# Kernel tuning notes

Measured on AMD Instinct MI355X. Metric: run time of the kernel, lower is better.

Reference implementation:

```python
import jax, jax.numpy as jnp
import numpy as np

SEQ_LEN = 2048   # configs.seq_len == h == KFSSM H
PRED_LEN = 720   # configs.pred_len == p
D_MODEL = 128    # configs.d_model == KFSSM N (complex state size N//2)
C_OUT = 64       # configs.c_out == channel dim of u
BATCH = 128


def setup_inputs() -> dict:
    key = jax.random.key(0)
    ks = jax.random.split(key, 12)
    H, n2, p = SEQ_LEN, D_MODEL // 2, PRED_LEN
    u = jax.random.normal(ks[0], (BATCH, SEQ_LEN, C_OUT), jnp.float32)
    x_mark_enc = jax.random.normal(ks[1], (BATCH, SEQ_LEN, 4), jnp.float32)
    x_dec = jax.random.normal(ks[2], (BATCH, PRED_LEN, C_OUT), jnp.float32)
    x_mark_dec = jax.random.normal(ks[3], (BATCH, PRED_LEN, 4), jnp.float32)
    # standard-normal noise; scaled by learned std inside reference (matches torch.normal(0, std))
    W_noise = jax.random.normal(ks[4], (BATCH, SEQ_LEN, C_OUT), jnp.float32)
    # Model params
    D = jax.random.normal(ks[5], (H,), jnp.float32)
    log_variance = jnp.log(1.0 + jax.random.uniform(ks[6], (1,), jnp.float32))
    # KFSSM params
    C_param = jax.random.normal(ks[7], (H, n2, 2), jnp.float32)  # view_as_real of complex C
    log_dt = (jax.random.uniform(ks[8], (H,), jnp.float32)
              * (np.log(0.1) - np.log(0.001)) + np.log(0.001))
    log_A_real = jnp.log(0.5 * jnp.ones((H, n2), jnp.float32))
    A_imag = np.pi * jnp.tile(jnp.arange(n2, dtype=jnp.float32)[None, :], (H, 1))
    # outporj: Linear(h -> 2p) then GLU(dim=2)
    proj_w = jax.random.normal(ks[9], (2 * p, H), jnp.float32) * 0.02
    proj_b = jnp.zeros((2 * p,), jnp.float32)
    return dict(u=u, x_mark_enc=x_mark_enc, x_dec=x_dec, x_mark_dec=x_mark_dec,
                W_noise=W_noise, D=D, log_variance=log_variance, C_param=C_param,
                log_dt=log_dt, log_A_real=log_A_real, A_imag=A_imag,
                proj_w=proj_w, proj_b=proj_b)


def _ssm_kernels(Nl, C_param, log_dt, log_A_real, A_imag):
    # KFSSM.forward(N=Nl): returns K, K2 of shape (H, Nl)
    dt = jnp.exp(log_dt)                              # (H,)
    C = C_param[..., 0] + 1j * C_param[..., 1]        # (H, n2)
    A = -jnp.exp(log_A_real) + 1j * A_imag            # (H, n2)
    ar = jnp.arange(Nl, dtype=log_dt.dtype)
    Bk = A[:, :1] * ar[None, :] * dt[:, None]         # (H, Nl) complex
    dtA = A * dt[:, None]                             # (H, n2)
    Kexp = jnp.exp(dtA[:, :, None] * ar[None, None, :])  # (H, n2, Nl)
    Cc = C * (jnp.exp(dtA) - 1.0) / A                 # (H, n2)
    K = 2.0 * jnp.einsum('hn,hnl->hl', Cc, Kexp).real # (H, Nl)
    K2 = 2.0 * (K * Bk).real                          # (H, Nl)
    return K, K2


def reference(u, x_mark_enc, x_dec, x_mark_dec, W_noise, D, log_variance,
              C_param, log_dt, log_A_real, A_imag, proj_w, proj_b):
    # instance normalization over time
    x_mean = jnp.mean(u, axis=1, keepdims=True)                  # (B,1,N)
    u0 = u - x_mean
    x_var = jnp.var(u0, axis=1, ddof=1, keepdims=True) + 1e-5    # unbiased, as torch.var
    un = u0 / jnp.sqrt(x_var)
    # Kalman process noise
    std = jnp.sqrt(jnp.exp(log_variance))                        # (1,)
    W = std * W_noise                                            # (B,L,N)
    l, Nch = un.shape[1], un.shape[2]
    nfft = 2 * l
    K, K2 = _ssm_kernels(Nch, C_param, log_dt, log_A_real, A_imag)  # (H=l, Nch)
    k_f = jnp.fft.rfft(K.T, n=nfft, axis=-1)                     # (Nch, l+1)
    k2_f = jnp.fft.rfft(K2.T, n=nfft, axis=-1)
    u_f = jnp.fft.rfft(jnp.transpose(un, (0, 2, 1)), n=nfft, axis=-1)   # (B,Nch,l+1)
    w_f = jnp.fft.rfft(jnp.transpose(W, (0, 2, 1)), n=nfft, axis=-1)
    y = (jnp.fft.irfft(u_f * k2_f, n=nfft, axis=-1)
         + jnp.fft.irfft(w_f * k_f, n=nfft, axis=-1))            # (B,Nch,2l)
    y = jnp.transpose(y, (0, 2, 1))[:, -l:, :] + un * D[:, None] # (B,l,Nch)
    # outporj: Linear(h->2p) over time axis, then GLU(dim=2); Dropout1d is identity at eval
    z = jnp.einsum('bnh,ph->bnp', jnp.transpose(y, (0, 2, 1)), proj_w) + proj_b  # (B,Nch,2p)
    a, b = jnp.split(z, 2, axis=2)
    y = jnp.transpose(a * jax.nn.sigmoid(b), (0, 2, 1))          # (B,p,Nch)
    y = y * jnp.sqrt(x_var) + x_mean
    return y[:, -PRED_LEN:, :]
```

## Files before the change

kernel.cpp:

```cpp
#include <hip/hip_runtime.h>
#include <math.h>

typedef unsigned short u16;
typedef unsigned int u32;
typedef __attribute__((ext_vector_type(8))) short short8;
typedef __attribute__((ext_vector_type(4))) float f32x4;

#define B_   128
#define L_   2048
#define C_   64
#define P_   720
#define P2_  1440
#define NPAD 1536
#define NFFT 4096
#define NROW (B_*C_)
#define TCHUNK 16

__device__ __forceinline__ u16 f2bf(float f) {
  union { float f; unsigned u; } x; x.f = f;
  unsigned r = x.u + 0x7fffu + ((x.u >> 16) & 1u);
  return (u16)(r >> 16);
}
__device__ __forceinline__ float bf2f_lo(u32 v) {
  union { unsigned u; float f; } x; x.u = v << 16; return x.f;
}
__device__ __forceinline__ float bf2f_hi(u32 v) {
  union { unsigned u; float f; } x; x.u = v & 0xffff0000u; return x.f;
}

__device__ __forceinline__ float2 cmul(float2 a, float2 b) {
  return make_float2(a.x * b.x - a.y * b.y, a.x * b.y + a.y * b.x);
}
__device__ __forceinline__ float2 cadd(float2 a, float2 b) { return make_float2(a.x + b.x, a.y + b.y); }
__device__ __forceinline__ float2 csub(float2 a, float2 b) { return make_float2(a.x - b.x, a.y - b.y); }

#define CSWAP(i, j) { float2 tt = a[i]; a[i] = a[j]; a[j] = tt; }

template<bool INV, bool HZ>
__device__ __forceinline__ void dft16(float2 a[16]) {
  const float S  = INV ? 1.f : -1.f;
  const float c1 = 0.9238795325112867f, s1 = 0.3826834323650898f, q2 = 0.7071067811865476f;
  const float2 W1 = make_float2( c1, S * s1), W2 = make_float2( q2, S * q2), W3 = make_float2( s1, S * c1);
  const float2 W5 = make_float2(-s1, S * c1), W6 = make_float2(-q2, S * q2), W7 = make_float2(-c1, S * s1);
  if (HZ) {
    a[8]  = a[0];
    a[9]  = cmul(a[1], W1);
    a[10] = cmul(a[2], W2);
    a[11] = cmul(a[3], W3);
    a[12] = make_float2(-S * a[4].y, S * a[4].x);
    a[13] = cmul(a[5], W5);
    a[14] = cmul(a[6], W6);
    a[15] = cmul(a[7], W7);
  } else {
    float2 t;
    t = csub(a[0], a[8]);  a[0] = cadd(a[0], a[8]);  a[8]  = t;
    t = csub(a[1], a[9]);  a[1] = cadd(a[1], a[9]);  a[9]  = cmul(t, W1);
    t = csub(a[2], a[10]); a[2] = cadd(a[2], a[10]); a[10] = cmul(t, W2);
    t = csub(a[3], a[11]); a[3] = cadd(a[3], a[11]); a[11] = cmul(t, W3);
    t = csub(a[4], a[12]); a[4] = cadd(a[4], a[12]); a[12] = make_float2(-S * t.y, S * t.x);
    t = csub(a[5], a[13]); a[5] = cadd(a[5], a[13]); a[13] = cmul(t, W5);
    t = csub(a[6], a[14]); a[6] = cadd(a[6], a[14]); a[14] = cmul(t, W6);
    t = csub(a[7], a[15]); a[7] = cadd(a[7], a[15]); a[15] = cmul(t, W7);
  }
#pragma unroll
  for (int h = 0; h < 16; h += 8) {
    float2 t;
    t = csub(a[h+0], a[h+4]); a[h+0] = cadd(a[h+0], a[h+4]); a[h+4] = t;
    t = csub(a[h+1], a[h+5]); a[h+1] = cadd(a[h+1], a[h+5]); a[h+5] = cmul(t, W2);
    t = csub(a[h+2], a[h+6]); a[h+2] = cadd(a[h+2], a[h+6]); a[h+6] = make_float2(-S * t.y, S * t.x);
    t = csub(a[h+3], a[h+7]); a[h+3] = cadd(a[h+3], a[h+7]); a[h+7] = cmul(t, W6);
  }
#pragma unroll
  for (int q = 0; q < 16; q += 4) {
    float2 t;
    t = csub(a[q+0], a[q+2]); a[q+0] = cadd(a[q+0], a[q+2]); a[q+2] = t;
    t = csub(a[q+1], a[q+3]); a[q+1] = cadd(a[q+1], a[q+3]); a[q+3] = make_float2(-S * t.y, S * t.x);
  }
#pragma unroll
  for (int p = 0; p < 16; p += 2) {
    float2 t = csub(a[p], a[p+1]); a[p] = cadd(a[p], a[p+1]); a[p+1] = t;
  }
  CSWAP(1, 8); CSWAP(2, 4); CSWAP(3, 12); CSWAP(5, 10); CSWAP(7, 14); CSWAP(11, 13);
}

__device__ __forceinline__ void twchain(float2 a[16], float2 w1) {
  float2 w2 = cmul(w1, w1);
  float2 w3 = cmul(w2, w1);
  float2 w4 = cmul(w2, w2);
  float2 w5 = cmul(w3, w2);
  float2 w6 = cmul(w3, w3);
  float2 w7 = cmul(w4, w3);
  float2 w8 = cmul(w4, w4);
  float2 w9 = cmul(w5, w4);
  float2 w10 = cmul(w5, w5);
  float2 w11 = cmul(w6, w5);
  float2 w12 = cmul(w6, w6);
  float2 w13 = cmul(w7, w6);
  float2 w14 = cmul(w7, w7);
  float2 w15 = cmul(w8, w7);
  a[1]  = cmul(a[1],  w1);  a[2]  = cmul(a[2],  w2);  a[3]  = cmul(a[3],  w3);
  a[4]  = cmul(a[4],  w4);  a[5]  = cmul(a[5],  w5);  a[6]  = cmul(a[6],  w6);
  a[7]  = cmul(a[7],  w7);  a[8]  = cmul(a[8],  w8);  a[9]  = cmul(a[9],  w9);
  a[10] = cmul(a[10], w10); a[11] = cmul(a[11], w11); a[12] = cmul(a[12], w12);
  a[13] = cmul(a[13], w13); a[14] = cmul(a[14], w14); a[15] = cmul(a[15], w15);
}

__device__ __forceinline__ void lds_wA(float2* X, const float2 r[16], int tid) {
  int base = (tid & 15) * 16 + ((tid >> 4) ^ ((tid & 7) << 1));
#pragma unroll
  for (int i = 0; i < 16; ++i) X[base + i * 256] = r[i];
}
__device__ __forceinline__ void lds_wB(float2* X, const float2 r[16], int tid) {
#pragma unroll
  for (int i = 0; i < 16; ++i)
    X[((tid & 0xF0) + i) * 16 + ((tid & 15) ^ ((i & 7) << 1))] = r[i];
}
__device__ __forceinline__ void lds_rd(const float2* X, float2 r[16], int tid) {
  const float4* X4 = (const float4*)X;
#pragma unroll
  for (int p = 0; p < 8; ++p) {
    float4 v = X4[tid * 8 + (p ^ (tid & 7))];
    r[2 * p]     = make_float2(v.x, v.y);
    r[2 * p + 1] = make_float2(v.z, v.w);
  }
}

__device__ __forceinline__ void fft_fwd_hz(float2 r[16], float2* X, int tid, const float2* twg) {
  dft16<false, true>(r);
  twchain(r, twg[tid]);
  lds_wA(X, r, tid);
  __syncthreads();
  lds_rd(X, r, tid);
  dft16<false, false>(r);
  twchain(r, twg[(tid & 15) << 4]);
  __syncthreads();
  lds_wB(X, r, tid);
  __syncthreads();
  lds_rd(X, r, tid);
  dft16<false, false>(r);
}

__device__ __forceinline__ void fft_inv(float2 r[16], float2* X, int tid, const float2* twg) {
  dft16<true, false>(r);
  __syncthreads();
  lds_wB(X, r, tid);
  __syncthreads();
  lds_rd(X, r, tid);
  float2 wb = twg[(tid & 15) << 4];
  twchain(r, make_float2(wb.x, -wb.y));
  dft16<true, false>(r);
  __syncthreads();
  lds_wA(X, r, tid);
  __syncthreads();
  lds_rd(X, r, tid);
  float2 wa = twg[tid];
  twchain(r, make_float2(wa.x, -wa.y));
  dft16<true, false>(r);
}

__global__ void k_twfill(float2* __restrict__ tw) {
  int k = threadIdx.x;
  double ang = -2.0 * 3.14159265358979323846 * (double)k / 4096.0;
  tw[k] = make_float2((float)cos(ang), (float)sin(ang));
}

__global__ void k_wconv(const float* __restrict__ pw, u16* __restrict__ wb) {
  size_t idx = (size_t)blockIdx.x * 256 + threadIdx.x;
  int n = (int)(idx >> 11);
  int k = (int)(idx & 2047);
  float v = (n < P2_) ? pw[(size_t)n * L_ + k] : 0.0f;
  wb[idx] = f2bf(v);
}

__global__ __launch_bounds__(256) void k_stats1(const float* __restrict__ u, float* __restrict__ ps,
                                                float* __restrict__ pq) {
  int blk = blockIdx.x;
  int b = blk >> 4, q = blk & 15;
  int tid = threadIdx.x;
  int c4 = tid & 15, g = tid >> 4;
  const float4* u4 = (const float4*)(u + ((size_t)b * L_ + q * 128) * C_);
  float4 s = make_float4(0.f, 0.f, 0.f, 0.f), sq = s;
#pragma unroll
  for (int i = 0; i < 8; ++i) {
    float4 v = u4[(size_t)(g + 16 * i) * 16 + c4];
    s.x += v.x; s.y += v.y; s.z += v.z; s.w += v.w;
    sq.x += v.x * v.x; sq.y += v.y * v.y; sq.z += v.z * v.z; sq.w += v.w * v.w;
  }
  __shared__ float4 sb[16][16], qb[16][16];
  sb[g][c4] = s; qb[g][c4] = sq;
  __syncthreads();
  if (g == 0) {
    float4 S = sb[0][c4], Q = qb[0][c4];
#pragma unroll
    for (int k = 1; k < 16; ++k) {
      float4 a = sb[k][c4], d = qb[k][c4];
      S.x += a.x; S.y += a.y; S.z += a.z; S.w += a.w;
      Q.x += d.x; Q.y += d.y; Q.z += d.z; Q.w += d.w;
    }
    ((float4*)ps)[blk * 16 + c4] = S;
    ((float4*)pq)[blk * 16 + c4] = Q;
  }
}

__global__ __launch_bounds__(256) void k_stats2(const float* __restrict__ ps, const float* __restrict__ pq,
                                                float4* __restrict__ mv) {
  int gid = blockIdx.x * 256 + threadIdx.x;
  int b = gid >> 6, c = gid & 63;
  float S = 0.f, Q = 0.f;
#pragma unroll
  for (int q = 0; q < 16; ++q) {
    S += ps[(size_t)(b * 16 + q) * 64 + c];
    Q += pq[(size_t)(b * 16 + q) * 64 + c];
  }
  float mean = S * (1.0f / 2048.0f);
  float var = (Q - S * S * (1.0f / 2048.0f)) * (1.0f / 2047.0f) + 1e-5f;
  float sv = sqrtf(var);
  mv[gid] = make_float4(mean, sv, 1.0f / sv, 0.0f);
}

__global__ __launch_bounds__(256) void k_ssmk(const float* __restrict__ Cp, const float* __restrict__ ldt,
                                              const float* __restrict__ lAr, const float* __restrict__ Aim,
                                              float2* __restrict__ kz) {
  int gid = blockIdx.x * 256 + threadIdx.x;
  int h = gid & 2047;
  int j = gid >> 11;
  float dt = expf(ldt[h]);
  float accx = 0.f;
  float Ar0 = 0.f;
  for (int n = 0; n < 64; ++n) {
    float Ar = -expf(lAr[h * 64 + n]);
    float Ai = Aim[h * 64 + n];
    if (n == 0) Ar0 = Ar;
    float dAr = Ar * dt, dAi = Ai * dt;
    float er = expf(dAr);
    float s1, c1; sincosf(dAi, &s1, &c1);
    float emr = er * c1 - 1.0f, emi = er * s1;
    float inv = 1.0f / (Ar * Ar + Ai * Ai);
    float qr = (emr * Ar + emi * Ai) * inv;
    float qi = (emi * Ar - emr * Ai) * inv;
    float cr = Cp[(size_t)(h * 64 + n) * 2];
    float ci = Cp[(size_t)(h * 64 + n) * 2 + 1];
    float ccr = cr * qr - ci * qi;
    float cci = cr * qi + ci * qr;
    float ej = expf(dAr * (float)j);
    float sj, cj; sincosf(dAi * (float)j, &sj, &cj);
    accx += ccr * (ej * cj) - cci * (ej * sj);
  }
  float K = 2.0f * accx;
  float K2 = 2.0f * K * (Ar0 * (float)j * dt);
  kz[(size_t)j * L_ + h] = make_float2(K2, -K);
}

__global__ __launch_bounds__(256) void k_packT(const float* __restrict__ u, const float* __restrict__ Wn,
                                               const float* __restrict__ lv, const float4* __restrict__ mv,
                                               u32* __restrict__ zu) {
  int b = blockIdx.x >> 5;
  int t0 = (blockIdx.x & 31) << 6;
  int tid = threadIdx.x;
  float stdn = sqrtf(__expf(lv[0]));
  __shared__ float2 tile[64][65];
  int c = tid & 63, r = tid >> 6;
  float4 m = mv[b * C_ + c];
#pragma unroll
  for (int i = 0; i < 16; ++i) {
    int t = t0 + i * 4 + r;
    size_t idx = ((size_t)b * L_ + t) * C_ + c;
    float uu = (u[idx] - m.x) * m.z;
    float ww = Wn[idx] * stdn;
    tile[i * 4 + r][c] = make_float2(uu, ww);
  }
  __syncthreads();
  int t = tid & 63, cb = tid >> 6;
#pragma unroll
  for (int i = 0; i < 16; ++i) {
    int c2 = i * 4 + cb;
    float2 v = tile[t][c2];
    zu[((size_t)(b * C_ + c2)) * L_ + t0 + t] = ((u32)f2bf(v.y) << 16) | (u32)f2bf(v.x);
  }
}

__global__ __launch_bounds__(256) void k_fftk(const float2* __restrict__ kz, const float2* __restrict__ twg,
                                              float2* __restrict__ G) {
  __shared__ float2 X[NFFT];
  int j = blockIdx.x, tid = threadIdx.x;
  float2 r[16];
#pragma unroll
  for (int n2 = 0; n2 < 8; ++n2) r[n2] = kz[(size_t)j * L_ + n2 * 256 + tid];
  fft_fwd_hz(r, X, tid, twg);
  const float sc = 1.0f / 8192.0f;
#pragma unroll
  for (int k0 = 0; k0 < 16; ++k0)
    G[(size_t)j * NFFT + k0 * 256 + tid] = make_float2(r[k0].x * sc, r[k0].y * sc);
}

__global__ __launch_bounds__(256) void k_fftmain(const u32* __restrict__ zu, const float2* __restrict__ twg,
                                                 const float2* __restrict__ G, const float* __restrict__ Dv,
                                                 u16* __restrict__ yT) {
  __shared__ float2 X[NFFT];
  int pair = blockIdx.x;
  int b = pair >> 5, j1 = pair & 31, j2 = j1 + 32;
  int row1 = b * 64 + j1, row2 = b * 64 + j2;
  int tid = threadIdx.x;
  float2 r[16], Y1[16];
  float usav1[8], usav2[8];
#pragma unroll
  for (int n2 = 0; n2 < 8; ++n2) {
    u32 v = zu[(size_t)row1 * L_ + n2 * 256 + tid];
    r[n2] = make_float2(bf2f_lo(v), bf2f_hi(v));
    usav1[n2] = r[n2].x;
  }
  fft_fwd_hz(r, X, tid, twg);
  const float2* G1 = G + (size_t)j1 * NFFT;
#pragma unroll
  for (int k0 = 0; k0 < 16; ++k0) Y1[k0] = cmul(r[k0], G1[k0 * 256 + tid]);
  __syncthreads();
#pragma unroll
  for (int n2 = 0; n2 < 8; ++n2) {
    u32 v = zu[(size_t)row2 * L_ + n2 * 256 + tid];
    r[n2] = make_float2(bf2f_lo(v), bf2f_hi(v));
    usav2[n2] = r[n2].x;
  }
  fft_fwd_hz(r, X, tid, twg);
  const float2* G2 = G + (size_t)j2 * NFFT;
#pragma unroll
  for (int k0 = 0; k0 < 16; ++k0) r[k0] = cmul(r[k0], G2[k0 * 256 + tid]);
  __syncthreads();
  int rr = (tid & 15) * 16 + (tid >> 4);
  int wsw = ((rr & 15) << 4) | (rr >> 4);
  int rp = (tid == 0) ? 0 : 256 - rr;
  int rsw = ((rp & 15) << 4) | (rp >> 4);
#pragma unroll
  for (int k0 = 0; k0 < 16; ++k0) {
    X[k0 * 256 + wsw] = make_float2(Y1[k0].x + r[k0].y, r[k0].x - Y1[k0].y);
  }
  __syncthreads();
#pragma unroll
  for (int k0 = 0; k0 < 16; ++k0) {
    int k0p = (tid == 0) ? ((16 - k0) & 15) : (15 - k0);
    float2 Tm = X[k0p * 256 + rsw];
    r[k0] = make_float2(Y1[k0].x - r[k0].y + Tm.x, Y1[k0].y + r[k0].x + Tm.y);
  }
  fft_inv(r, X, tid, twg);
#pragma unroll
  for (int n2 = 8; n2 < 16; ++n2) {
    int t = (n2 - 8) * 256 + tid;
    float d = Dv[t];
    yT[(size_t)row1 * L_ + t] = f2bf(r[n2].x + usav1[n2 - 8] * d);
    yT[(size_t)row2 * L_ + t] = f2bf(r[n2].y + usav2[n2 - 8] * d);
  }
}

__device__ __forceinline__ int lds_ix(int row, int slot) {
  return row * 32 + ((slot ^ ((row >> 1) & 3)) << 3);
}

__global__ __launch_bounds__(256) void k_gemm(const u16* __restrict__ A, const u16* __restrict__ B,
                                              float* __restrict__ Cmat) {
  __shared__ u16 As[128 * 32];
  __shared__ u16 Bs[128 * 32];
  const int K = L_, N = NPAD;
  int tid = threadIdx.x;
  int bid = blockIdx.x;
  int swz = (bid & 7) * 96 + (bid >> 3);
  int bm = swz % 64, bn = swz / 64;
  int wave = tid >> 6, lane = tid & 63;
  int wm = (wave >> 1) << 6, wn = (wave & 1) << 6;
  int lr = lane & 15, lk = lane >> 4;
  int trow = tid >> 2, tslot = tid & 3;
  const u16* Ag = A + (size_t)(bm * 128 + trow) * K + tslot * 8;
  const u16* Bg = B + (size_t)(bn * 128 + trow) * K + tslot * 8;
  f32x4 acc[4][4] = {};
  uint4 pa0 = *(const uint4*)(Ag);
  uint4 pa1 = *(const uint4*)(Ag + (size_t)64 * K);
  uint4 pb0 = *(const uint4*)(Bg);
  uint4 pb1 = *(const uint4*)(Bg + (size_t)64 * K);
  for (int kt = 0; kt < K; kt += 32) {
    __syncthreads();
    *(uint4*)&As[lds_ix(trow, tslot)] = pa0;
    *(uint4*)&As[lds_ix(trow + 64, tslot)] = pa1;
    *(uint4*)&Bs[lds_ix(trow, tslot)] = pb0;
    *(uint4*)&Bs[lds_ix(trow + 64, tslot)] = pb1;
    __syncthreads();
    if (kt + 32 < K) {
      pa0 = *(const uint4*)(Ag + kt + 32);
      pa1 = *(const uint4*)(Ag + (size_t)64 * K + kt + 32);
      pb0 = *(const uint4*)(Bg + kt + 32);
      pb1 = *(const uint4*)(Bg + (size_t)64 * K + kt + 32);
    }
    short8 af[4], bf[4];
#pragma unroll
    for (int i2 = 0; i2 < 4; ++i2) af[i2] = *(const short8*)&As[lds_ix(wm + i2 * 16 + lr, lk)];
#pragma unroll
    for (int j2 = 0; j2 < 4; ++j2) bf[j2] = *(const short8*)&Bs[lds_ix(wn + j2 * 16 + lr, lk)];
#pragma unroll
    for (int i2 = 0; i2 < 4; ++i2)
#pragma unroll
      for (int j2 = 0; j2 < 4; ++j2)
        acc[i2][j2] = __builtin_amdgcn_mfma_f32_16x16x32_bf16(af[i2], bf[j2], acc[i2][j2], 0, 0, 0);
  }
#pragma unroll
  for (int i2 = 0; i2 < 4; ++i2)
#pragma unroll
    for (int j2 = 0; j2 < 4; ++j2)
#pragma unroll
      for (int r = 0; r < 4; ++r)
        Cmat[(size_t)(bm * 128 + wm + i2 * 16 + lk * 4 + r) * N + bn * 128 + wn + j2 * 16 + lr] =
            acc[i2][j2][r];
}

__global__ __launch_bounds__(256) void k_epi(const float* __restrict__ z, const float* __restrict__ pb,
                                             const float4* __restrict__ mv, float* __restrict__ out) {
  int b = blockIdx.x / 23;
  int p0 = (blockIdx.x % 23) * 32;
  int tid = threadIdx.x;
  __shared__ float tile[64][33];
  int pp = tid & 31, ci = tid >> 5;
  for (int cc = ci; cc < 64; cc += 8) {
    int p = p0 + pp;
    float val = 0.f;
    if (p < P_) {
      size_t rowb = (size_t)(b * C_ + cc) * NPAD;
      float a = z[rowb + p] + pb[p];
      float g = z[rowb + P_ + p] + pb[P_ + p];
      float4 m = mv[b * C_ + cc];
      val = a * (1.0f / (1.0f + __expf(-g))) * m.y + m.x;
    }
    tile[cc][pp] = val;
  }
  __syncthreads();
  int c2 = tid & 63, pi = tid >> 6;
  for (int q = pi; q < 32; q += 4) {
    int p = p0 + q;
    if (p < P_) out[((size_t)b * P_ + p) * C_ + c2] = tile[c2][q];
  }
}

extern "C" void kernel_launch(void* const* d_in, const int* in_sizes, int n_in,
                              void* d_out, int out_size, void* d_ws, size_t ws_size,
                              hipStream_t stream) {
  const float* u   = (const float*)d_in[0];
  const float* Wn  = (const float*)d_in[4];
  const float* Dv  = (const float*)d_in[5];
  const float* lv  = (const float*)d_in[6];
  const float* Cp  = (const float*)d_in[7];
  const float* ldt = (const float*)d_in[8];
  const float* lAr = (const float*)d_in[9];
  const float* Aim = (const float*)d_in[10];
  const float* pw  = (const float*)d_in[11];
  const float* pb  = (const float*)d_in[12];
  float* out = (float*)d_out;
  char* ws = (char*)d_ws;

  float2* tw = (float2*)(ws + 0);
  float4* mv = (float4*)(ws + (64 << 10));
  float2* G  = (float2*)(ws + (1 << 20));
  float2* kz = (float2*)(ws + (3 << 20));
  u16*    Wb = (u16*)   (ws + (4 << 20));
  float*  ps = (float*) (ws + (10 << 20));
  float*  pq = (float*) (ws + (10 << 20) + (512 << 10));
  u16*    yT = (u16*)   (ws + (16 << 20));
  u32*    zu = (u32*)   (ws + ((size_t)48 << 20));
  float*  zz = (float*) (ws + ((size_t)112 << 20));

  k_twfill<<<1, 256, 0, stream>>>(tw);
  k_wconv<<<(NPAD * L_) / 256, 256, 0, stream>>>(pw, Wb);
  k_stats1<<<B_ * TCHUNK, 256, 0, stream>>>(u, ps, pq);
  k_stats2<<<(B_ * C_) / 256, 256, 0, stream>>>(ps, pq, mv);
  k_ssmk<<<(C_ * L_) / 256, 256, 0, stream>>>(Cp, ldt, lAr, Aim, kz);
  k_packT<<<B_ * (L_ / 64), 256, 0, stream>>>(u, Wn, lv, mv, zu);
  k_fftk<<<C_, 256, 0, stream>>>(kz, tw, G);
  k_fftmain<<<NROW / 2, 256, 0, stream>>>(zu, tw, G, Dv, yT);
  k_gemm<<<64 * (NPAD / 128), 256, 0, stream>>>(yT, Wb, zz);
  k_epi<<<B_ * 23, 256, 0, stream>>>(zz, pb, mv, out);
}
```

Before: 344.7 us.

## Fuse GLU epilogue into GEMM via interleaved weights; pack FFT intermediate to bf16

The projection weight rows are interleaved so that each gate column sits next to its value column. The GEMM epilogue can then apply bias, sigmoid gating and de-normalisation with a lane shuffle, stage the results in LDS and write the final transposed output directly. This removes the separate epilogue kernel and the round trip of the large fp32 intermediate matrix through memory. Separately, the first FFT row's product is held in registers as packed bf16 to cut register pressure in the FFT kernel, at some precision cost.

```diff
diff --git a/kernel.cpp b/kernel.cpp
--- a/kernel.cpp
+++ b/kernel.cpp
@@ -168,7 +168,12 @@
   size_t idx = (size_t)blockIdx.x * 256 + threadIdx.x;
   int n = (int)(idx >> 11);
   int k = (int)(idx & 2047);
-  float v = (n < P2_) ? pw[(size_t)n * L_ + k] : 0.0f;
+  int q = n >> 1;
+  float v = 0.f;
+  if (q < P_) {
+    int p = (n & 1) ? (P_ + q) : q;
+    v = pw[(size_t)p * L_ + k];
+  }
   wb[idx] = f2bf(v);
 }
 
@@ -301,7 +306,8 @@
   int b = pair >> 5, j1 = pair & 31, j2 = j1 + 32;
   int row1 = b * 64 + j1, row2 = b * 64 + j2;
   int tid = threadIdx.x;
-  float2 r[16], Y1[16];
+  float2 r[16];
+  u32 Y1p[16];
   float usav1[8], usav2[8];
 #pragma unroll
   for (int n2 = 0; n2 < 8; ++n2) {
@@ -312,7 +318,10 @@
   fft_fwd_hz(r, X, tid, twg);
   const float2* G1 = G + (size_t)j1 * NFFT;
 #pragma unroll
-  for (int k0 = 0; k0 < 16; ++k0) Y1[k0] = cmul(r[k0], G1[k0 * 256 + tid]);
+  for (int k0 = 0; k0 < 16; ++k0) {
+    float2 y = cmul(r[k0], G1[k0 * 256 + tid]);
+    Y1p[k0] = ((u32)f2bf(y.y) << 16) | (u32)f2bf(y.x);
+  }
   __syncthreads();
 #pragma unroll
   for (int n2 = 0; n2 < 8; ++n2) {
@@ -331,14 +340,15 @@
   int rsw = ((rp & 15) << 4) | (rp >> 4);
 #pragma unroll
   for (int k0 = 0; k0 < 16; ++k0) {
-    X[k0 * 256 + wsw] = make_float2(Y1[k0].x + r[k0].y, r[k0].x - Y1[k0].y);
+    X[k0 * 256 + wsw] = make_float2(bf2f_lo(Y1p[k0]) + r[k0].y, r[k0].x - bf2f_hi(Y1p[k0]));
   }
   __syncthreads();
 #pragma unroll
   for (int k0 = 0; k0 < 16; ++k0) {
     int k0p = (tid == 0) ? ((16 - k0) & 15) : (15 - k0);
     float2 Tm = X[k0p * 256 + rsw];
-    r[k0] = make_float2(Y1[k0].x - r[k0].y + Tm.x, Y1[k0].y + r[k0].x + Tm.y);
+    r[k0] = make_float2(bf2f_lo(Y1p[k0]) - r[k0].y + Tm.x,
+                        bf2f_hi(Y1p[k0]) + r[k0].x + Tm.y);
   }
   fft_inv(r, X, tid, twg);
 #pragma unroll
@@ -355,10 +365,12 @@
 }
 
 __global__ __launch_bounds__(256) void k_gemm(const u16* __restrict__ A, const u16* __restrict__ B,
-                                              float* __restrict__ Cmat) {
+                                              const float* __restrict__ pb, const float4* __restrict__ mv,
+                                              float* __restrict__ out) {
   __shared__ u16 As[128 * 32];
   __shared__ u16 Bs[128 * 32];
-  const int K = L_, N = NPAD;
+  __shared__ float ob[32 * 132];
+  const int K = L_;
   int tid = threadIdx.x;
   int bid = blockIdx.x;
   int swz = (bid & 7) * 96 + (bid >> 3);
@@ -398,40 +410,47 @@
       for (int j2 = 0; j2 < 4; ++j2)
         acc[i2][j2] = __builtin_amdgcn_mfma_f32_16x16x32_bf16(af[i2], bf[j2], acc[i2][j2], 0, 0, 0);
   }
-#pragma unroll
-  for (int i2 = 0; i2 < 4; ++i2)
-#pragma unroll
-    for (int j2 = 0; j2 < 4; ++j2)
-#pragma unroll
-      for (int r = 0; r < 4; ++r)
-        Cmat[(size_t)(bm * 128 + wm + i2 * 16 + lk * 4 + r) * N + bn * 128 + wn + j2 * 16 + lr] =
-            acc[i2][j2][r];
-}
-
-__global__ __launch_bounds__(256) void k_epi(const float* __restrict__ z, const float* __restrict__ pb,
-                                             const float4* __restrict__ mv, float* __restrict__ out) {
-  int b = blockIdx.x / 23;
-  int p0 = (blockIdx.x % 23) * 32;
-  int tid = threadIdx.x;
-  __shared__ float tile[64][33];
-  int pp = tid & 31, ci = tid >> 5;
-  for (int cc = ci; cc < 64; cc += 8) {
-    int p = p0 + pp;
-    float val = 0.f;
-    if (p < P_) {
-      size_t rowb = (size_t)(b * C_ + cc) * NPAD;
-      float a = z[rowb + p] + pb[p];
-      float g = z[rowb + P_ + p] + pb[P_ + p];
-      float4 m = mv[b * C_ + cc];
-      val = a * (1.0f / (1.0f + __expf(-g))) * m.y + m.x;
+  int col_lo = wn + lr;
+  for (int chunk = 0; chunk < 2; ++chunk) {
+    __syncthreads();
+#pragma unroll
+    for (int j2c = 0; j2c < 2; ++j2c) {
+      int j2 = chunk * 2 + j2c;
+      int col = col_lo + j2 * 16;
+      int nglob = bn * 128 + col;
+      int q = nglob >> 1;
+      float bias = 0.f;
+      if (q < P_) bias = pb[(nglob & 1) ? (P_ + q) : q];
+      int qloc = col >> 1;
+      int s = (qloc & 15) | ((qloc >> 5) << 4);
+#pragma unroll
+      for (int i2 = 0; i2 < 4; ++i2) {
+        int row = wm + i2 * 16 + lk * 4;
+        float res[4];
+#pragma unroll
+        for (int rgi = 0; rgi < 4; ++rgi) {
+          float val = acc[i2][j2][rgi] + bias;
+          float other = __shfl_xor(val, 1);
+          float4 m = mv[bm * 128 + row + rgi];
+          res[rgi] = val * (1.0f / (1.0f + __expf(-other))) * m.y + m.x;
+        }
+        if (!(lane & 1)) {
+          *(float4*)&ob[s * 132 + row] = make_float4(res[0], res[1], res[2], res[3]);
+        }
+      }
     }
-    tile[cc][pp] = val;
-  }
-  __syncthreads();
-  int c2 = tid & 63, pi = tid >> 6;
-  for (int q = pi; q < 32; q += 4) {
-    int p = p0 + q;
-    if (p < P_) out[((size_t)b * P_ + p) * C_ + c2] = tile[c2][q];
+    __syncthreads();
+    int c = tid & 63, sl4 = tid >> 6;
+    for (int rd = 0; rd < 16; ++rd) {
+      int slice = rd * 4 + sl4;
+      int s = slice >> 1, bb = slice & 1;
+      int qloc = (s & 15) + chunk * 16 + ((s >> 4) << 5);
+      int qglob = bn * 64 + qloc;
+      if (qglob < P_) {
+        int bg = bm * 2 + bb;
+        out[((size_t)bg * P_ + qglob) * 64 + c] = ob[s * 132 + bb * 64 + c];
+      }
+    }
   }
 }
 
@@ -460,7 +479,6 @@
   float*  pq = (float*) (ws + (10 << 20) + (512 << 10));
   u16*    yT = (u16*)   (ws + (16 << 20));
   u32*    zu = (u32*)   (ws + ((size_t)48 << 20));
-  float*  zz = (float*) (ws + ((size_t)112 << 20));
 
   k_twfill<<<1, 256, 0, stream>>>(tw);
   k_wconv<<<(NPAD * L_) / 256, 256, 0, stream>>>(pw, Wb);
@@ -470,6 +488,5 @@
   k_packT<<<B_ * (L_ / 64), 256, 0, stream>>>(u, Wn, lv, mv, zu);
   k_fftk<<<C_, 256, 0, stream>>>(kz, tw, G);
   k_fftmain<<<NROW / 2, 256, 0, stream>>>(zu, tw, G, Dv, yT);
-  k_gemm<<<64 * (NPAD / 128), 256, 0, stream>>>(yT, Wb, zz);
-  k_epi<<<B_ * 23, 256, 0, stream>>>(zz, pb, mv, out);
-}
+  k_gemm<<<64 * (NPAD / 128), 256, 0, stream>>>(yT, Wb, pb, mv, out);
+}
```

New measurement: 351.2 us. No clear change (+1.9%).
